# Performance work log

Hardware: AMD Instinct MI355X
Metric: run time of the kernel (lower is better)

The kernel has to match this reference:

```python
import jax, jax.numpy as jnp
import numpy as np

N_NODES = 100000
N_EDGES = 640000
HIDDEN = 128
EPS = 1e-6


def setup_inputs() -> dict:
    key = jax.random.key(0)
    k_x, k_w, k_a, k_e = jax.random.split(key, 4)
    x = jax.random.normal(k_x, (N_NODES, HIDDEN), dtype=jnp.float32)
    W = jax.random.normal(k_w, (HIDDEN, HIDDEN), dtype=jnp.float32) / np.sqrt(HIDDEN)
    b = jnp.zeros((HIDDEN,), dtype=jnp.float32)
    att_w = jax.random.normal(k_a, (1, 2 * HIDDEN), dtype=jnp.float32) / np.sqrt(2 * HIDDEN)
    norm_w = jnp.ones((HIDDEN,), dtype=jnp.float32)
    norm_b = jnp.zeros((HIDDEN,), dtype=jnp.float32)
    e = jax.random.randint(k_e, (N_EDGES, 2), 0, N_NODES, dtype=jnp.int64)
    return {"x": x, "W": W, "b": b, "att_w": att_w, "norm_w": norm_w, "norm_b": norm_b, "e": e}


def reference(x, W, b, att_w, norm_w, norm_b, e):
    n_nodes = x.shape[0]
    src, dst = e[:, 0], e[:, 1]
    # Edge gather + shared linear on both endpoints: [E, D]
    m = x[src] @ W.T + b
    s = x[dst] @ W.T + b
    # Attention score per edge: leaky_relu(concat @ w^T), then exp -> [E, 1]
    a = jnp.exp(jax.nn.leaky_relu(jnp.concatenate((m, s), axis=1) @ att_w.T, negative_slope=0.2))
    # NOTE: faithful to the original: this weighted message sum is computed
    # but then overwritten (dead code in the source module).
    _unused = jax.ops.segment_sum(a * m, dst, num_segments=n_nodes)
    # Normalizer: sum of attention weights per destination node -> [N, 1]
    n = jax.ops.segment_sum(a, dst, num_segments=n_nodes)
    h = jax.nn.relu(x / jnp.where(n == 0.0, 1.0, n))
    # Residual + RMSNorm (per-row, with affine weight and bias, eps=1e-6)
    y = h + x
    inv_rms = jax.lax.rsqrt(jnp.mean(y * y, axis=-1, keepdims=True) + EPS)
    return norm_w * (y * inv_rms) + norm_b
```

## Files before the change

kernel.cpp:

```cpp
#include <hip/hip_runtime.h>

#define N_NODES 100000
#define N_EDGES 640000
#define HIDDEN  128
#define EPS     1e-6f

__global__ void precompute_uvc(const float* __restrict__ W,
                               const float* __restrict__ b,
                               const float* __restrict__ att_w,
                               float* __restrict__ u,
                               float* __restrict__ v,
                               float* __restrict__ c) {
    __shared__ float su_s[4][HIDDEN];
    __shared__ float sv_s[4][HIDDEN];
    int k     = threadIdx.x & 127;
    int chunk = threadIdx.x >> 7;

    float su = 0.f, sv = 0.f;
    #pragma unroll
    for (int jj = 0; jj < 32; ++jj) {
        int j = chunk * 32 + jj;
        float w = W[j * HIDDEN + k];
        su += att_w[j] * w;
        sv += att_w[HIDDEN + j] * w;
    }
    su_s[chunk][k] = su;
    sv_s[chunk][k] = sv;

    if (threadIdx.x < 64) {
        int t0 = threadIdx.x, t1 = threadIdx.x + 64;
        float t = att_w[t0] * b[t0] + att_w[HIDDEN + t0] * b[t0]
                + att_w[t1] * b[t1] + att_w[HIDDEN + t1] * b[t1];
        #pragma unroll
        for (int off = 32; off > 0; off >>= 1) t += __shfl_xor(t, off);
        if (threadIdx.x == 0) *c = t;
    }

    __syncthreads();
    if (chunk == 0) {
        u[k] = su_s[0][k] + su_s[1][k] + su_s[2][k] + su_s[3][k];
        v[k] = sv_s[0][k] + sv_s[1][k] + sv_s[2][k] + sv_s[3][k];
    }
}

__global__ void node_dots(const float* __restrict__ x,
                          const float* __restrict__ u,
                          const float* __restrict__ v,
                          float* __restrict__ p,
                          float* __restrict__ q,
                          float* __restrict__ nacc) {
    int gid  = blockIdx.x * blockDim.x + threadIdx.x;
    int wave = gid >> 6;
    int lane = threadIdx.x & 63;
    int half = lane >> 5;
    int sub  = lane & 31;
    int node = wave * 2 + half;
    if (node >= N_NODES) return;

    float4 xv = ((const float4*)(x + (size_t)node * HIDDEN))[sub];
    float4 uv = ((const float4*)u)[sub];
    float4 vv = ((const float4*)v)[sub];

    float sp = xv.x * uv.x + xv.y * uv.y + xv.z * uv.z + xv.w * uv.w;
    float sq = xv.x * vv.x + xv.y * vv.y + xv.z * vv.z + xv.w * vv.w;
    #pragma unroll
    for (int off = 16; off > 0; off >>= 1) {
        sp += __shfl_xor(sp, off);
        sq += __shfl_xor(sq, off);
    }
    if (sub == 0) {
        p[node]    = sp;
        q[node]    = sq;
        nacc[node] = 0.f;
    }
}

__global__ void edge_kernel(const int* __restrict__ e,
                            const float* __restrict__ p,
                            const float* __restrict__ q,
                            const float* __restrict__ c,
                            float* __restrict__ nacc) {
    int eid = blockIdx.x * blockDim.x + threadIdx.x;
    if (eid >= N_EDGES) return;
    int2 ed = ((const int2*)e)[eid];
    float score = p[ed.x] + q[ed.y] + c[0];
    float lr = score > 0.f ? score : 0.2f * score;
    atomicAdd(&nacc[ed.y], __expf(lr) == __expf(lr) ? expf(lr) : expf(lr));
}

__global__ void final_kernel(const float* __restrict__ x,
                             const float* __restrict__ nacc,
                             const float* __restrict__ norm_w,
                             const float* __restrict__ norm_b,
                             float* __restrict__ out) {
    int gid  = blockIdx.x * blockDim.x + threadIdx.x;
    int wave = gid >> 6;
    int lane = threadIdx.x & 63;
    int half = lane >> 5;
    int sub  = lane & 31;
    int node = wave * 2 + half;
    if (node >= N_NODES) return;

    float nn = nacc[node];
    float inv_n = 1.f / (nn == 0.f ? 1.f : nn);

    float4 xv = ((const float4*)(x + (size_t)node * HIDDEN))[sub];
    float4 y;
    {
        float h;
        h = xv.x * inv_n; h = h > 0.f ? h : 0.f; y.x = h + xv.x;
        h = xv.y * inv_n; h = h > 0.f ? h : 0.f; y.y = h + xv.y;
        h = xv.z * inv_n; h = h > 0.f ? h : 0.f; y.z = h + xv.z;
        h = xv.w * inv_n; h = h > 0.f ? h : 0.f; y.w = h + xv.w;
    }

    float ss = y.x * y.x + y.y * y.y + y.z * y.z + y.w * y.w;
    #pragma unroll
    for (int off = 16; off > 0; off >>= 1) ss += __shfl_xor(ss, off);
    float inv_rms = rsqrtf(ss * (1.f / HIDDEN) + EPS);

    float4 wv = ((const float4*)norm_w)[sub];
    float4 bv = ((const float4*)norm_b)[sub];
    float4 ov;
    ov.x = wv.x * (y.x * inv_rms) + bv.x;
    ov.y = wv.y * (y.y * inv_rms) + bv.y;
    ov.z = wv.z * (y.z * inv_rms) + bv.z;
    ov.w = wv.w * (y.w * inv_rms) + bv.w;
    ((float4*)(out + (size_t)node * HIDDEN))[sub] = ov;
}

extern "C" void kernel_launch(void* const* d_in, const int* in_sizes, int n_in,
                              void* d_out, int out_size, void* d_ws, size_t ws_size,
                              hipStream_t stream) {
    const float* x      = (const float*)d_in[0];
    const float* W      = (const float*)d_in[1];
    const float* b      = (const float*)d_in[2];
    const float* att_w  = (const float*)d_in[3];
    const float* norm_w = (const float*)d_in[4];
    const float* norm_b = (const float*)d_in[5];
    const int*   e      = (const int*)d_in[6];
    float* out = (float*)d_out;

    float* ws = (float*)d_ws;
    float* u    = ws;
    float* v    = ws + 128;
    float* c    = ws + 256;
    float* p    = ws + 1024;
    float* q    = p + N_NODES;
    float* nacc = q + N_NODES;

    precompute_uvc<<<1, 512, 0, stream>>>(W, b, att_w, u, v, c);

    {
        int blocks = (N_NODES + 7) / 8;
        node_dots<<<blocks, 256, 0, stream>>>(x, u, v, p, q, nacc);
    }
    {
        int blocks = (N_EDGES + 255) / 256;
        edge_kernel<<<blocks, 256, 0, stream>>>(e, p, q, c, nacc);
    }
    {
        int blocks = (N_NODES + 7) / 8;
        final_kernel<<<blocks, 256, 0, stream>>>(x, nacc, norm_w, norm_b, out);
    }
}
```

Baseline: 158.4 us.

## Fuse all GAT stages into one persistent cooperative kernel with grid syncs

```diff
diff --git a/kernel.cpp b/kernel.cpp
--- a/kernel.cpp
+++ b/kernel.cpp
@@ -1,132 +1,139 @@
 #include <hip/hip_runtime.h>
+#include <hip/hip_cooperative_groups.h>
+
+namespace cg = cooperative_groups;
 
 #define N_NODES 100000
 #define N_EDGES 640000
 #define HIDDEN  128
 #define EPS     1e-6f
 
-__global__ void precompute_uvc(const float* __restrict__ W,
-                               const float* __restrict__ b,
-                               const float* __restrict__ att_w,
-                               float* __restrict__ u,
-                               float* __restrict__ v,
-                               float* __restrict__ c) {
-    __shared__ float su_s[4][HIDDEN];
-    __shared__ float sv_s[4][HIDDEN];
-    int k     = threadIdx.x & 127;
-    int chunk = threadIdx.x >> 7;
+__global__ __launch_bounds__(256, 4) void fused_gat(
+    const float* __restrict__ x,
+    const float* __restrict__ W,
+    const float* __restrict__ b,
+    const float* __restrict__ att_w,
+    const float* __restrict__ norm_w,
+    const float* __restrict__ norm_b,
+    const int*   __restrict__ e,
+    float* __restrict__ p,
+    float* __restrict__ q,
+    float* __restrict__ nacc,
+    float* __restrict__ out)
+{
+    cg::grid_group grid = cg::this_grid();
 
-    float su = 0.f, sv = 0.f;
-    #pragma unroll
-    for (int jj = 0; jj < 32; ++jj) {
-        int j = chunk * 32 + jj;
-        float w = W[j * HIDDEN + k];
-        su += att_w[j] * w;
-        sv += att_w[HIDDEN + j] * w;
-    }
-    su_s[chunk][k] = su;
-    sv_s[chunk][k] = sv;
+    __shared__ float part_u[2][HIDDEN];
+    __shared__ float part_v[2][HIDDEN];
+    __shared__ __align__(16) float uv_s[2 * HIDDEN];
+    __shared__ float c_s;
 
-    if (threadIdx.x < 64) {
-        int t0 = threadIdx.x, t1 = threadIdx.x + 64;
-        float t = att_w[t0] * b[t0] + att_w[HIDDEN + t0] * b[t0]
-                + att_w[t1] * b[t1] + att_w[HIDDEN + t1] * b[t1];
-        #pragma unroll
-        for (int off = 32; off > 0; off >>= 1) t += __shfl_xor(t, off);
-        if (threadIdx.x == 0) *c = t;
+    const int tid = threadIdx.x;
+
+    {
+        const int k  = tid & 127;
+        const int jh = tid >> 7;
+        float su = 0.f, sv = 0.f;
+        #pragma unroll 8
+        for (int jj = 0; jj < 64; ++jj) {
+            int j = jh * 64 + jj;
+            float w = W[j * HIDDEN + k];
+            su += att_w[j] * w;
+            sv += att_w[HIDDEN + j] * w;
+        }
+        part_u[jh][k] = su;
+        part_v[jh][k] = sv;
+
+        if (tid < 64) {
+            int t0 = tid, t1 = tid + 64;
+            float t = (att_w[t0] + att_w[HIDDEN + t0]) * b[t0]
+                    + (att_w[t1] + att_w[HIDDEN + t1]) * b[t1];
+            #pragma unroll
+            for (int off = 32; off > 0; off >>= 1) t += __shfl_xor(t, off);
+            if (tid == 0) c_s = t;
+        }
+        __syncthreads();
+        if (tid < HIDDEN) {
+            uv_s[tid]          = part_u[0][tid] + part_u[1][tid];
+            uv_s[HIDDEN + tid] = part_v[0][tid] + part_v[1][tid];
+        }
+        __syncthreads();
     }
 
-    __syncthreads();
-    if (chunk == 0) {
-        u[k] = su_s[0][k] + su_s[1][k] + su_s[2][k] + su_s[3][k];
-        v[k] = sv_s[0][k] + sv_s[1][k] + sv_s[2][k] + sv_s[3][k];
-    }
-}
+    const int lane = tid & 63;
+    const int half = lane >> 5;
+    const int sub  = lane & 31;
+    const float4 u4 = ((const float4*)uv_s)[sub];
+    const float4 v4 = ((const float4*)(uv_s + HIDDEN))[sub];
+    const float  cc = c_s;
 
-__global__ void node_dots(const float* __restrict__ x,
-                          const float* __restrict__ u,
-                          const float* __restrict__ v,
-                          float* __restrict__ p,
-                          float* __restrict__ q,
-                          float* __restrict__ nacc) {
-    int gid  = blockIdx.x * blockDim.x + threadIdx.x;
-    int wave = gid >> 6;
-    int lane = threadIdx.x & 63;
-    int half = lane >> 5;
-    int sub  = lane & 31;
-    int node = wave * 2 + half;
-    if (node >= N_NODES) return;
+    const int gsize  = (int)(gridDim.x * blockDim.x);
+    const int gtid   = (int)(blockIdx.x * blockDim.x) + tid;
+    const int nwaves = gsize >> 6;
+    const int wid    = gtid >> 6;
 
-    float4 xv = ((const float4*)(x + (size_t)node * HIDDEN))[sub];
-    float4 uv = ((const float4*)u)[sub];
-    float4 vv = ((const float4*)v)[sub];
-
-    float sp = xv.x * uv.x + xv.y * uv.y + xv.z * uv.z + xv.w * uv.w;
-    float sq = xv.x * vv.x + xv.y * vv.y + xv.z * vv.z + xv.w * vv.w;
-    #pragma unroll
-    for (int off = 16; off > 0; off >>= 1) {
-        sp += __shfl_xor(sp, off);
-        sq += __shfl_xor(sq, off);
-    }
-    if (sub == 0) {
-        p[node]    = sp;
-        q[node]    = sq;
-        nacc[node] = 0.f;
-    }
-}
-
-__global__ void edge_kernel(const int* __restrict__ e,
-                            const float* __restrict__ p,
-                            const float* __restrict__ q,
-                            const float* __restrict__ c,
-                            float* __restrict__ nacc) {
-    int eid = blockIdx.x * blockDim.x + threadIdx.x;
-    if (eid >= N_EDGES) return;
-    int2 ed = ((const int2*)e)[eid];
-    float score = p[ed.x] + q[ed.y] + c[0];
-    float lr = score > 0.f ? score : 0.2f * score;
-    atomicAdd(&nacc[ed.y], __expf(lr) == __expf(lr) ? expf(lr) : expf(lr));
-}
-
-__global__ void final_kernel(const float* __restrict__ x,
-                             const float* __restrict__ nacc,
-                             const float* __restrict__ norm_w,
-                             const float* __restrict__ norm_b,
-                             float* __restrict__ out) {
-    int gid  = blockIdx.x * blockDim.x + threadIdx.x;
-    int wave = gid >> 6;
-    int lane = threadIdx.x & 63;
-    int half = lane >> 5;
-    int sub  = lane & 31;
-    int node = wave * 2 + half;
-    if (node >= N_NODES) return;
-
-    float nn = nacc[node];
-    float inv_n = 1.f / (nn == 0.f ? 1.f : nn);
-
-    float4 xv = ((const float4*)(x + (size_t)node * HIDDEN))[sub];
-    float4 y;
-    {
-        float h;
-        h = xv.x * inv_n; h = h > 0.f ? h : 0.f; y.x = h + xv.x;
-        h = xv.y * inv_n; h = h > 0.f ? h : 0.f; y.y = h + xv.y;
-        h = xv.z * inv_n; h = h > 0.f ? h : 0.f; y.z = h + xv.z;
-        h = xv.w * inv_n; h = h > 0.f ? h : 0.f; y.w = h + xv.w;
+    for (int node = wid * 2 + half; node < N_NODES; node += nwaves * 2) {
+        float4 xv = ((const float4*)(x + (size_t)node * HIDDEN))[sub];
+        float sp = xv.x * u4.x + xv.y * u4.y + xv.z * u4.z + xv.w * u4.w;
+        float sq = xv.x * v4.x + xv.y * v4.y + xv.z * v4.z + xv.w * v4.w;
+        #pragma unroll
+        for (int off = 16; off > 0; off >>= 1) {
+            sp += __shfl_xor(sp, off);
+            sq += __shfl_xor(sq, off);
+        }
+        if (sub == 0) {
+            p[node]    = sp;
+            q[node]    = sq;
+            nacc[node] = 0.f;
+        }
     }
 
-    float ss = y.x * y.x + y.y * y.y + y.z * y.z + y.w * y.w;
-    #pragma unroll
-    for (int off = 16; off > 0; off >>= 1) ss += __shfl_xor(ss, off);
-    float inv_rms = rsqrtf(ss * (1.f / HIDDEN) + EPS);
+    __threadfence();
+    grid.sync();
+    __threadfence();
 
-    float4 wv = ((const float4*)norm_w)[sub];
-    float4 bv = ((const float4*)norm_b)[sub];
-    float4 ov;
-    ov.x = wv.x * (y.x * inv_rms) + bv.x;
-    ov.y = wv.y * (y.y * inv_rms) + bv.y;
-    ov.z = wv.z * (y.z * inv_rms) + bv.z;
-    ov.w = wv.w * (y.w * inv_rms) + bv.w;
-    ((float4*)(out + (size_t)node * HIDDEN))[sub] = ov;
+    for (int i = gtid; i < N_EDGES / 2; i += gsize) {
+        int4 ed = ((const int4*)e)[i];
+        float s0 = p[ed.x] + q[ed.y] + cc;
+        float s1 = p[ed.z] + q[ed.w] + cc;
+        s0 = s0 > 0.f ? s0 : 0.2f * s0;
+        s1 = s1 > 0.f ? s1 : 0.2f * s1;
+        atomicAdd(&nacc[ed.y], expf(s0));
+        atomicAdd(&nacc[ed.w], expf(s1));
+    }
+
+    __threadfence();
+    grid.sync();
+    __threadfence();
+
+    for (int node = wid * 2 + half; node < N_NODES; node += nwaves * 2) {
+        float nn    = nacc[node];
+        float inv_n = 1.f / (nn == 0.f ? 1.f : nn);
+
+        float4 xv = ((const float4*)(x + (size_t)node * HIDDEN))[sub];
+        float4 y;
+        {
+            float h;
+            h = xv.x * inv_n; h = h > 0.f ? h : 0.f; y.x = h + xv.x;
+            h = xv.y * inv_n; h = h > 0.f ? h : 0.f; y.y = h + xv.y;
+            h = xv.z * inv_n; h = h > 0.f ? h : 0.f; y.z = h + xv.z;
+            h = xv.w * inv_n; h = h > 0.f ? h : 0.f; y.w = h + xv.w;
+        }
+
+        float ss = y.x * y.x + y.y * y.y + y.z * y.z + y.w * y.w;
+        #pragma unroll
+        for (int off = 16; off > 0; off >>= 1) ss += __shfl_xor(ss, off);
+        float inv_rms = rsqrtf(ss * (1.f / HIDDEN) + EPS);
+
+        float4 wv = ((const float4*)norm_w)[sub];
+        float4 bv = ((const float4*)norm_b)[sub];
+        float4 ov;
+        ov.x = wv.x * (y.x * inv_rms) + bv.x;
+        ov.y = wv.y * (y.y * inv_rms) + bv.y;
+        ov.z = wv.z * (y.z * inv_rms) + bv.z;
+        ov.w = wv.w * (y.w * inv_rms) + bv.w;
+        ((float4*)(out + (size_t)node * HIDDEN))[sub] = ov;
+    }
 }
 
 extern "C" void kernel_launch(void* const* d_in, const int* in_sizes, int n_in,
@@ -141,26 +148,28 @@
     const int*   e      = (const int*)d_in[6];
     float* out = (float*)d_out;
 
-    float* ws = (float*)d_ws;
-    float* u    = ws;
-    float* v    = ws + 128;
-    float* c    = ws + 256;
-    float* p    = ws + 1024;
-    float* q    = p + N_NODES;
-    float* nacc = q + N_NODES;
+    float* ws   = (float*)d_ws;
+    float* p    = ws;
+    float* q    = ws + N_NODES;
+    float* nacc = ws + 2 * N_NODES;
 
-    precompute_uvc<<<1, 512, 0, stream>>>(W, b, att_w, u, v, c);
+    static int s_grid = 0;
+    if (s_grid == 0) {
+        int nb = 0;
+        hipError_t err =
+            hipOccupancyMaxActiveBlocksPerMultiprocessor(&nb, fused_gat, 256, 0);
+        if (err != hipSuccess || nb < 1) nb = 4;
+        s_grid = nb * 256;
+        if (s_grid > 2048) s_grid = 2048;
+        if (s_grid < 256)  s_grid = 256;
+    }
 
-    {
-        int blocks = (N_NODES + 7) / 8;
-        node_dots<<<blocks, 256, 0, stream>>>(x, u, v, p, q, nacc);
-    }
-    {
-        int blocks = (N_EDGES + 255) / 256;
-        edge_kernel<<<blocks, 256, 0, stream>>>(e, p, q, c, nacc);
-    }
-    {
-        int blocks = (N_NODES + 7) / 8;
-        final_kernel<<<blocks, 256, 0, stream>>>(x, nacc, norm_w, norm_b, out);
-    }
+    void* args[] = {
+        (void*)&x, (void*)&W, (void*)&b, (void*)&att_w,
+        (void*)&norm_w, (void*)&norm_b, (void*)&e,
+        (void*)&p, (void*)&q, (void*)&nacc, (void*)&out
+    };
+    hipLaunchCooperativeKernel((const void*)fused_gat,
+                               dim3(s_grid), dim3(256),
+                               args, 0, stream);
 }
```

After: 528.7 us. 234% more time.
